# Optimization experiments

Measured on AMD Instinct MI355X. Metric: run time of the kernel, lower is better.

## Reference

```python
import jax, jax.numpy as jnp
import numpy as np

CONF_THRES = 0.5   # self.conf_thres
NMS_THRES = 0.5    # self.nms_thres
PRE_NMS = 2048     # candidates kept before pairwise IoU
MAX_DET = 300      # padded detections returned per image
MAX_WH = 4096.0    # class-offset trick so NMS is per-class
IMG_SIZE = 416.0   # self.img_size; boxes_scale (416,416)->(416,416) => scale 1


def xywh2xyxy(b):
    xy, wh = b[..., :2], b[..., 2:4]
    return jnp.concatenate([xy - wh * 0.5, xy + wh * 0.5], axis=-1)


def pairwise_iou(boxes):
    # boxes: [K,4] xyxy -> [K,K] IoU
    area = (boxes[:, 2] - boxes[:, 0]) * (boxes[:, 3] - boxes[:, 1])
    lt = jnp.maximum(boxes[:, None, :2], boxes[None, :, :2])
    rb = jnp.minimum(boxes[:, None, 2:], boxes[None, :, 2:])
    wh = jnp.clip(rb - lt, 0.0)
    inter = wh[..., 0] * wh[..., 1]
    return inter / (area[:, None] + area[None, :] - inter + 1e-16)


def nms_single(pred):
    # pred: [N,85] = xywh(4) + objectness(1) + class scores(80)
    boxes = xywh2xyxy(pred[:, :4])
    obj = pred[:, 4]
    cls_scores = pred[:, 5:] * obj[:, None]        # conf = obj * class prob
    conf = jnp.max(cls_scores, axis=-1)
    cls_id = jnp.argmax(cls_scores, axis=-1)
    valid = obj >= CONF_THRES                      # confidence threshold filter
    score = jnp.where(valid, conf, -1.0)

    order = jnp.argsort(-score)[:PRE_NMS]          # sort desc, keep top PRE_NMS
    boxes_s = boxes[order]
    score_s = score[order]
    cls_s = cls_id[order]
    valid_s = valid[order]

    # per-class NMS via coordinate offset by class id
    off = cls_s.astype(boxes_s.dtype) * MAX_WH
    iou = pairwise_iou(boxes_s + off[:, None])     # [PRE_NMS, PRE_NMS]

    def body(keep, i):
        suppressed = jnp.any(keep & (iou[:, i] > NMS_THRES))
        k = valid_s[i] & ~suppressed
        return keep.at[i].set(k), k

    keep, _ = jax.lax.scan(body, jnp.zeros(PRE_NMS, dtype=bool), jnp.arange(PRE_NMS))

    final_score = jnp.where(keep, score_s, -1.0)
    top = jnp.argsort(-final_score)[:MAX_DET]
    kb, ks, kc, km = boxes_s[top], score_s[top], cls_s[top], keep[top]

    scale = IMG_SIZE / 416.0                       # boxes_scale (identity here)
    det = jnp.concatenate(
        [kb * scale, ks[:, None], kc[:, None].astype(kb.dtype)], axis=-1)
    return jnp.where(km[:, None], det, 0.0)        # [MAX_DET, 6] padded


def setup_inputs() -> dict:
    key = jax.random.key(0)
    predictions = jax.random.uniform(key, (16, 10647, 85), dtype=jnp.float32)
    return {"predictions": predictions}


def reference(predictions):
    # detections per image: [x1,y1,x2,y2,score,class], zero-padded to MAX_DET
    return jax.vmap(nms_single)(predictions)  # [B, MAX_DET, 6]
```

## Files before the change

### kernel.cpp

```cpp
#include <hip/hip_runtime.h>
#include <hip/hip_bf16.h>
#include <stdint.h>

typedef unsigned long long u64;
typedef unsigned int u32;
typedef unsigned short u16;

#define NANCH 10647
#define NBATCH 16
#define NSORT 16384
#define NSEL 2048
#define NWORD 32
#define NCLS 80
#define CONF_T 0.5f
#define NMS_T 0.5f
#define MAXDET 300
#define MAXWH 4096.0f
#define CANDCAP 10688
#define PART 1344

__global__ __launch_bounds__(1024) void k_zero(u32* __restrict__ p, int nwords) {
    for (int i = threadIdx.x; i < nwords; i += 1024) p[i] = 0;
}

__global__ __launch_bounds__(256) void k_prep(const float* __restrict__ pred,
                                              u64* __restrict__ keys,
                                              float4* __restrict__ boxes,
                                              int* __restrict__ cls,
                                              float* __restrict__ score,
                                              u32* __restrict__ ghist) {
    __shared__ float sm[128 * 85];
    __shared__ u32 ph[256];
    int b = blockIdx.y;
    int a0 = blockIdx.x * 128;
    int na = NANCH - a0; if (na > 128) na = 128;
    const float* src = pred + ((size_t)b * NANCH + a0) * 85;
    int tot = na * 85;
    ph[threadIdx.x] = 0;
    {
        size_t srcaddr = (size_t)src;
        int shift = (int)((srcaddr & 15) >> 2);
        const float4* A = (const float4*)(srcaddr & ~(size_t)15);
        int nvec = (tot + shift + 3) >> 2;
        for (int j = threadIdx.x; j < nvec; j += 256) {
            float4 v = A[j];
            int base = 4 * j - shift;
            if (base >= 0 && base + 3 < tot) {
                sm[base] = v.x; sm[base + 1] = v.y;
                sm[base + 2] = v.z; sm[base + 3] = v.w;
            } else {
                if (base >= 0 && base < tot)     sm[base]     = v.x;
                if (base + 1 >= 0 && base + 1 < tot) sm[base + 1] = v.y;
                if (base + 2 >= 0 && base + 2 < tot) sm[base + 2] = v.z;
                if (base + 3 >= 0 && base + 3 < tot) sm[base + 3] = v.w;
            }
        }
    }
    __syncthreads();
    int t = threadIdx.x;
    u64 kk = 0;
    if (t < na) {
        const float* s = &sm[t * 85];
        float x = s[0], y = s[1], w = s[2], h = s[3], obj = s[4];
        float best = s[5] * obj; int arg = 0;
        #pragma unroll
        for (int c = 1; c < 80; ++c) {
            float v = s[5 + c] * obj;
            if (v > best) { best = v; arg = c; }
        }
        bool valid = obj >= CONF_T;
        float sc = valid ? best : -1.0f;
        int a = a0 + t;
        float4 bx;
        bx.x = x - w * 0.5f; bx.y = y - h * 0.5f;
        bx.z = x + w * 0.5f; bx.w = y + h * 0.5f;
        size_t o = (size_t)b * NANCH + a;
        boxes[o] = bx;
        cls[o] = arg;
        score[o] = sc;
        u32 u = __float_as_uint(sc);
        u32 v = (u & 0x80000000u) ? ~u : (u | 0x80000000u);
        u32 hi = ~v;
        kk = ((u64)hi << 32) | (u32)a;
        keys[(size_t)b * NSORT + a] = kk;
    }
    u32 bin = (t < na) ? (u32)(kk >> 56) : 0xFFFFFFFFu;
    int lane = t & 63;
    u64 rem = __ballot(t < na);
    while (rem) {
        int srcl = __ffsll((long long)rem) - 1;
        u32 lb = __shfl(bin, srcl);
        u64 same = __ballot(bin == lb) & rem;
        if (lane == srcl) atomicAdd(&ph[lb], (u32)__popcll(same));
        rem &= ~same;
    }
    __syncthreads();
    if (ph[threadIdx.x]) atomicAdd(&ghist[(size_t)b * 256 + threadIdx.x], ph[threadIdx.x]);
}

__global__ __launch_bounds__(1024) void k_scan(const u64* __restrict__ keys,
                                               const u32* __restrict__ ghist,
                                               u64* __restrict__ gsk,
                                               u64* __restrict__ gcand,
                                               u32* __restrict__ gcnt,
                                               u32* __restrict__ gcandcnt) {
    __shared__ u32 hist[256];
    __shared__ u32 hsc[256];
    __shared__ u32 s_D0;
    __shared__ u32 wcs[16], wcc[16];
    __shared__ u32 s_gbs, s_gbc;
    int b = blockIdx.y;
    int part = blockIdx.x;
    int tid = threadIdx.x;
    int lane = tid & 63, wv = tid >> 6;
    u64 below = (1ULL << lane) - 1ULL;
    const u64* KB = keys + (size_t)b * NSORT;

    if (tid < 256) hist[tid] = ghist[(size_t)b * 256 + tid];
    __syncthreads();
    if (tid < 64) {
        u32 h0 = hist[tid*4], h1 = hist[tid*4+1], h2 = hist[tid*4+2], h3 = hist[tid*4+3];
        u32 loc = h0 + h1 + h2 + h3;
        u32 p = loc;
        #pragma unroll
        for (int o = 1; o < 64; o <<= 1) { u32 t2 = __shfl_up(p, o); if (lane >= o) p += t2; }
        u32 base = p - loc;
        hsc[tid*4]   = base + h0;
        hsc[tid*4+1] = base + h0 + h1;
        hsc[tid*4+2] = base + h0 + h1 + h2;
        hsc[tid*4+3] = base + h0 + h1 + h2 + h3;
    }
    __syncthreads();
    if (tid < 256) {
        u32 inc = hsc[tid], cb = inc - hist[tid];
        if (cb < NSEL && NSEL <= inc) s_D0 = tid;
    }
    __syncthreads();
    u32 D0 = s_D0;

    u64 kk0 = 0, kk1 = 0;
    bool s0 = false, s1 = false, c0 = false, c1 = false;
    {
        int off = tid, i = part * PART + off;
        bool inb = (off < PART) && (i < NANCH);
        kk0 = inb ? KB[i] : 0ULL;
        u32 top = (u32)(kk0 >> 56);
        s0 = inb && (top < D0); c0 = inb && (top == D0);
    }
    {
        int off = 1024 + tid, i = part * PART + off;
        bool inb = (off < PART) && (i < NANCH);
        kk1 = inb ? KB[i] : 0ULL;
        u32 top = (u32)(kk1 >> 56);
        s1 = inb && (top < D0); c1 = inb && (top == D0);
    }
    u64 bs0 = __ballot(s0), bs1 = __ballot(s1);
    u64 bc0 = __ballot(c0), bc1 = __ballot(c1);
    if (lane == 0) {
        wcs[wv] = (u32)(__popcll(bs0) + __popcll(bs1));
        wcc[wv] = (u32)(__popcll(bc0) + __popcll(bc1));
    }
    __syncthreads();
    if (tid < 16) {
        u32 vs = wcs[tid], vc = wcc[tid];
        u32 ps = vs, pc = vc;
        #pragma unroll
        for (int o = 1; o < 16; o <<= 1) {
            u32 ts = __shfl_up(ps, o);
            u32 tc = __shfl_up(pc, o);
            if (tid >= o) { ps += ts; pc += tc; }
        }
        wcs[tid] = ps - vs;
        wcc[tid] = pc - vc;
        if (tid == 15) {
            s_gbs = ps ? atomicAdd(&gcnt[b], ps) : 0u;
            s_gbc = pc ? atomicAdd(&gcandcnt[b], pc) : 0u;
        }
    }
    __syncthreads();
    u64* SKB = gsk + (size_t)b * NSEL;
    u64* CDB = gcand + (size_t)b * CANDCAP;
    u32 base_s = s_gbs + wcs[wv];
    u32 base_c = s_gbc + wcc[wv];
    if (s0) SKB[base_s + __popcll(bs0 & below)] = kk0;
    if (s1) SKB[base_s + __popcll(bs0) + __popcll(bs1 & below)] = kk1;
    if (c0) CDB[base_c + __popcll(bc0 & below)] = kk0;
    if (c1) CDB[base_c + __popcll(bc0) + __popcll(bc1 & below)] = kk1;
}

__global__ __launch_bounds__(1024) void k_fin(const u64* __restrict__ gsk,
                                              const u64* __restrict__ gcand,
                                              const u32* __restrict__ gcnt,
                                              const u32* __restrict__ gcandcnt,
                                              u64* __restrict__ gskey) {
    __shared__ u64 sk[NSEL];
    __shared__ u64 cand[CANDCAP];
    __shared__ u32 hist[256];
    __shared__ u32 hsc[256];
    __shared__ u64 s_red[16];
    __shared__ u32 s_D, s_rank, s_cnt, s_cand;

    int b = blockIdx.x;
    int tid = threadIdx.x;
    int lane = tid & 63;
    u64 below = (1ULL << lane) - 1ULL;

    u32 skn = gcnt[b];
    u32 cn0 = gcandcnt[b];
    if (tid == 0) { s_cnt = skn; s_rank = NSEL - skn; s_cand = cn0; }
    for (int i = tid; i < NSEL; i += 1024)
        sk[i] = (i < (int)skn) ? gsk[(size_t)b * NSEL + i] : ~0ULL;
    for (u32 i = tid; i < cn0; i += 1024)
        cand[i] = gcand[(size_t)b * CANDCAP + i];
    __syncthreads();

    const int shifts2[5] = {48, 40, 32, 8, 0};
    for (int rr = 0; ; ++rr) {
        u32 cn = s_cand, r = s_rank;
        if (r == cn || rr == 5) {
            for (u32 i0 = 0; i0 < cn; i0 += 1024) {
                u32 i = i0 + tid;
                bool take = i < cn;
                u64 kk = take ? cand[i] : 0ULL;
                u64 bt = __ballot(take);
                u32 base = 0;
                if (lane == 0 && bt) base = atomicAdd(&s_cnt, (u32)__popcll(bt));
                base = __shfl(base, 0);
                if (take) sk[base + __popcll(bt & below)] = kk;
            }
            break;
        }
        if (r == 1) {
            u64 best = ~0ULL;
            for (u32 i = tid; i < cn; i += 1024) { u64 kk = cand[i]; if (kk < best) best = kk; }
            #pragma unroll
            for (int o = 32; o > 0; o >>= 1) {
                u64 other = __shfl_down(best, o);
                if (other < best) best = other;
            }
            if (lane == 0) s_red[tid >> 6] = best;
            __syncthreads();
            if (tid == 0) {
                u64 m = s_red[0];
                for (int w2 = 1; w2 < 16; ++w2) if (s_red[w2] < m) m = s_red[w2];
                sk[atomicAdd(&s_cnt, 1u)] = m;
            }
            break;
        }
        int shift = shifts2[rr];
        if (tid < 256) hist[tid] = 0;
        __syncthreads();
        for (u32 i = tid; i < cn; i += 1024)
            atomicAdd(&hist[(u32)(cand[i] >> shift) & 0xFFu], 1u);
        __syncthreads();
        if (tid < 64) {
            u32 h0 = hist[tid*4], h1 = hist[tid*4+1], h2 = hist[tid*4+2], h3 = hist[tid*4+3];
            u32 loc = h0 + h1 + h2 + h3;
            u32 p = loc;
            #pragma unroll
            for (int o = 1; o < 64; o <<= 1) { u32 t2 = __shfl_up(p, o); if (lane >= o) p += t2; }
            u32 base = p - loc;
            hsc[tid*4]   = base + h0;
            hsc[tid*4+1] = base + h0 + h1;
            hsc[tid*4+2] = base + h0 + h1 + h2;
            hsc[tid*4+3] = base + h0 + h1 + h2 + h3;
        }
        __syncthreads();
        if (tid < 256) {
            u32 inc = hsc[tid], cb = inc - hist[tid];
            if (cb < r && r <= inc) { s_D = tid; s_rank = r - cb; }
        }
        __syncthreads();
        u32 D = s_D;
        u64 vv[11]; bool vb[11];
        #pragma unroll
        for (int it = 0; it < 11; ++it) {
            u32 i = tid + it * 1024;
            vb[it] = (i < cn);
            vv[it] = vb[it] ? cand[i] : 0ULL;
        }
        __syncthreads();
        if (tid == 0) s_cand = 0;
        __syncthreads();
        #pragma unroll
        for (int it = 0; it < 11; ++it) {
            u32 dg = (u32)(vv[it] >> shift) & 0xFFu;
            bool tk = vb[it] && (dg < D);
            u64 bt = __ballot(tk);
            u32 base = 0;
            if (lane == 0 && bt) base = atomicAdd(&s_cnt, (u32)__popcll(bt));
            base = __shfl(base, 0);
            if (tk) sk[base + __popcll(bt & below)] = vv[it];
        }
        #pragma unroll
        for (int it = 0; it < 11; ++it) {
            u32 dg = (u32)(vv[it] >> shift) & 0xFFu;
            bool tk = vb[it] && (dg == D);
            u64 bt = __ballot(tk);
            u32 base = 0;
            if (lane == 0 && bt) base = atomicAdd(&s_cand, (u32)__popcll(bt));
            base = __shfl(base, 0);
            if (tk) cand[base + __popcll(bt & below)] = vv[it];
        }
        __syncthreads();
    }
    __syncthreads();

    {
        int w = tid >> 6, l = lane;
        int base = w * 128;
        u64 a = sk[base + l], c = sk[base + 64 + l];
        #pragma unroll
        for (int k = 2; k <= 128; k <<= 1) {
            for (int j = k >> 1; j > 0; j >>= 1) {
                if (j == 64) {
                    bool dir = (((base + l) & k) == 0);
                    u64 lo = a < c ? a : c;
                    u64 hi = a < c ? c : a;
                    a = dir ? lo : hi;
                    c = dir ? hi : lo;
                } else {
                    bool up_ = (l & j) != 0;
                    bool dira = (((base + l) & k) == 0);
                    bool dirc = (((base + 64 + l) & k) == 0);
                    u64 pa = __shfl_xor(a, j);
                    u64 pc = __shfl_xor(c, j);
                    a = (up_ == dira) ? (a > pa ? a : pa) : (a < pa ? a : pa);
                    c = (up_ == dirc) ? (c > pc ? c : pc) : (c < pc ? c : pc);
                }
            }
        }
        sk[base + l] = a; sk[base + 64 + l] = c;
        __syncthreads();
        for (int k = 256; k <= NSEL; k <<= 1) {
            for (int j = k >> 1; j >= 128; j >>= 1) {
                int n = tid;
                int i = ((n & ~(j - 1)) << 1) | (n & (j - 1));
                int l2 = i | j;
                u64 x = sk[i], y = sk[l2];
                bool up2 = ((i & k) == 0);
                if ((x > y) == up2) { sk[i] = y; sk[l2] = x; }
                __syncthreads();
            }
            a = sk[base + l]; c = sk[base + 64 + l];
            bool dirk = ((base & k) == 0);
            {
                u64 lo = a < c ? a : c;
                u64 hi = a < c ? c : a;
                a = dirk ? lo : hi;
                c = dirk ? hi : lo;
            }
            #pragma unroll
            for (int j = 32; j > 0; j >>= 1) {
                bool up_ = (l & j) != 0;
                u64 pa = __shfl_xor(a, j);
                u64 pc = __shfl_xor(c, j);
                a = (up_ == dirk) ? (a > pa ? a : pa) : (a < pa ? a : pa);
                c = (up_ == dirk) ? (c > pc ? c : pc) : (c < pc ? c : pc);
            }
            sk[base + l] = a; sk[base + 64 + l] = c;
            __syncthreads();
        }
    }

    for (int i = tid; i < NSEL; i += 1024) gskey[(size_t)b * NSEL + i] = sk[i];
}

__global__ __launch_bounds__(256) void k_gather(const u64* __restrict__ gskey,
                                                const float4* __restrict__ boxes,
                                                const int* __restrict__ cls,
                                                const float* __restrict__ score,
                                                float4* __restrict__ sel_box,
                                                float4* __restrict__ sel_sbox,
                                                float* __restrict__ sel_area,
                                                float* __restrict__ sel_score,
                                                int* __restrict__ sel_cls) {
    int b = blockIdx.y;
    int r = blockIdx.x * 256 + threadIdx.x;
    u64 key = gskey[(size_t)b * NSEL + r];
    int a = (int)(key & 0xFFFFFFFFu);
    if ((unsigned)a >= NANCH) a = 0;
    size_t src = (size_t)b * NANCH + a;
    float4 bx = boxes[src];
    int c = cls[src];
    float sc = score[src];
    float off = (float)c * MAXWH;
    float4 sb;
    sb.x = bx.x + off; sb.y = bx.y + off;
    sb.z = bx.z + off; sb.w = bx.w + off;
    float area = (sb.z - sb.x) * (sb.w - sb.y);
    size_t o = (size_t)b * NSEL + r;
    sel_box[o] = bx; sel_sbox[o] = sb; sel_area[o] = area;
    sel_score[o] = sc; sel_cls[o] = c;
}

__global__ __launch_bounds__(1024) void k_cnms(const float4* __restrict__ sel_sbox,
                                               const float* __restrict__ sel_area,
                                               const int* __restrict__ sel_cls,
                                               const float* __restrict__ sel_score,
                                               u64* __restrict__ gkeep) {
    __shared__ u16 wmem[16][NSEL];
    __shared__ u64 wkeep[16][NWORD];

    int b = blockIdx.y;
    int cg = blockIdx.x;
    int lane = threadIdx.x & 63, wv = threadIdx.x >> 6;
    int c = cg * 16 + wv;
    size_t bb = (size_t)b * NSEL;
    const int* CL = sel_cls + bb;
    const float* SC = sel_score + bb;
    u64 below = (1ULL << lane) - 1ULL;

    int n = 0;
    for (int ch = 0; ch < NWORD; ++ch) {
        int i = ch * 64 + lane;
        bool pred = (CL[i] == c) && (SC[i] >= 0.0f);
        u64 bal = __ballot(pred);
        if (pred) wmem[wv][n + __popcll(bal & below)] = (u16)i;
        n += __popcll(bal);
    }

    for (int c0 = 0; c0 < n; c0 += 64) {
        int chunkn = n - c0; if (chunkn > 64) chunkn = 64;
        bool mv = lane < chunkn;
        int q = mv ? (int)wmem[wv][c0 + lane] : 0;
        float4 bq = sel_sbox[bb + q];
        float aq = sel_area[bb + q];

        bool hit = false;
        for (int j = 0; j < c0; ++j) {
            if (!((wkeep[wv][j >> 6] >> (j & 63)) & 1ULL)) continue;
            int p = (int)wmem[wv][j];
            float4 bp = sel_sbox[bb + p];
            float ap = sel_area[bb + p];
            float ltx = fmaxf(bp.x, bq.x), lty = fmaxf(bp.y, bq.y);
            float rbx = fminf(bp.z, bq.z), rby = fminf(bp.w, bq.w);
            float ww = fmaxf(rbx - ltx, 0.0f), hh = fmaxf(rby - lty, 0.0f);
            float inter = ww * hh;
            hit = hit || (mv && (inter / (ap + aq - inter + 1e-16f) > NMS_T));
        }
        u64 avail = __ballot(mv && !hit);

        u64 Rt = 0;
        for (int t = 0; t < chunkn; ++t) {
            int p = (int)wmem[wv][c0 + t];
            float4 bp = sel_sbox[bb + p];
            float ap = sel_area[bb + p];
            float ltx = fmaxf(bp.x, bq.x), lty = fmaxf(bp.y, bq.y);
            float rbx = fminf(bp.z, bq.z), rby = fminf(bp.w, bq.w);
            float ww = fmaxf(rbx - ltx, 0.0f), hh = fmaxf(rby - lty, 0.0f);
            float inter = ww * hh;
            u64 row = __ballot(mv && (inter / (ap + aq - inter + 1e-16f) > NMS_T));
            if (lane == t) Rt = row;
        }

        u64 U = avail, kept = 0;
        while (U) {
            bool inU = ((U >> lane) & 1ULL) != 0ULL;
            u64 newk = __ballot(inU && ((Rt & U & below) == 0ULL));
            u64 killed = __ballot((Rt & newk) != 0ULL);
            kept |= newk;
            U &= ~(newk | killed);
        }
        if (lane == 0) wkeep[wv][c0 >> 6] = kept;
        if ((kept >> lane) & 1ULL)
            atomicOr(&gkeep[(size_t)b * NWORD + (q >> 6)], 1ULL << (q & 63));
    }
}

__global__ __launch_bounds__(64) void k_out(const u64* __restrict__ gkeep,
                                            const float4* __restrict__ sel_box,
                                            const float* __restrict__ sel_score,
                                            const int* __restrict__ sel_cls,
                                            float* __restrict__ out) {
    int b = blockIdx.x;
    int lane = threadIdx.x;
    const float* SC = sel_score + (size_t)b * NSEL;
    u64 kreg = (lane < NWORD) ? gkeep[(size_t)b * NWORD + lane] : 0ULL;

    int cnt = (lane < NWORD) ? __popcll(kreg) : 0;
    int pre = cnt;
    #pragma unroll
    for (int dd = 1; dd < 64; dd <<= 1) {
        int o = __shfl_up(pre, dd);
        if (lane >= dd) pre += o;
    }
    int total = __shfl(pre, 63);
    int base = pre - cnt;
    float* OUT = out + (size_t)b * MAXDET * 6;
    if (lane < NWORD) {
        u64 m = kreg;
        int rr = 0;
        while (m) {
            int t = __ffsll((long long)m) - 1;
            m &= m - 1;
            int slot = base + rr; ++rr;
            if (slot < MAXDET) {
                int i = lane * 64 + t;
                size_t src = (size_t)b * NSEL + i;
                float4 bx = sel_box[src];
                float sc = SC[i];
                int c = sel_cls[src];
                float* o6 = OUT + slot * 6;
                o6[0] = bx.x; o6[1] = bx.y; o6[2] = bx.z; o6[3] = bx.w;
                o6[4] = sc; o6[5] = (float)c;
            }
        }
    }
    int start = total > MAXDET ? MAXDET : total;
    for (int s = start + lane; s < MAXDET; s += 64) {
        float* o6 = OUT + s * 6;
        o6[0] = 0.0f; o6[1] = 0.0f; o6[2] = 0.0f;
        o6[3] = 0.0f; o6[4] = 0.0f; o6[5] = 0.0f;
    }
}

extern "C" void kernel_launch(void* const* d_in, const int* in_sizes, int n_in,
                              void* d_out, int out_size, void* d_ws, size_t ws_size,
                              hipStream_t stream) {
    const float* pred = (const float*)d_in[0];
    float* out = (float*)d_out;

    char* ws = (char*)d_ws;
    size_t off = 0;
    auto alloc = [&](size_t bytes) -> void* {
        void* p = ws + off;
        off += (bytes + 255) & ~(size_t)255;
        return p;
    };

    u64*    keys      = (u64*)   alloc((size_t)NBATCH * NSORT * 8);
    float4* boxes     = (float4*)alloc((size_t)NBATCH * NANCH * 16);
    int*    cls       = (int*)   alloc((size_t)NBATCH * NANCH * 4);
    float*  score     = (float*) alloc((size_t)NBATCH * NANCH * 4);
    float4* sel_box   = (float4*)alloc((size_t)NBATCH * NSEL * 16);
    float4* sel_sbox  = (float4*)alloc((size_t)NBATCH * NSEL * 16);
    float*  sel_area  = (float*) alloc((size_t)NBATCH * NSEL * 4);
    float*  sel_score = (float*) alloc((size_t)NBATCH * NSEL * 4);
    int*    sel_cls   = (int*)   alloc((size_t)NBATCH * NSEL * 4);
    u64*    gsk       = (u64*)   alloc((size_t)NBATCH * NSEL * 8);
    u64*    gcand     = (u64*)   alloc((size_t)NBATCH * CANDCAP * 8);
    u64*    gskey     = (u64*)   alloc((size_t)NBATCH * NSEL * 8);
    u64*    gkeep     = (u64*)   alloc((size_t)NBATCH * NWORD * 8);
    u32*    ghist     = (u32*)   alloc((size_t)NBATCH * 256 * 4);
    u32*    gcnt      = (u32*)   alloc((size_t)NBATCH * 4);
    u32*    gcandcnt  = (u32*)   alloc((size_t)NBATCH * 4);

    size_t zbytes = (char*)(gcandcnt + NBATCH) - (char*)gkeep;
    k_zero<<<1, 1024, 0, stream>>>((u32*)gkeep, (int)(zbytes / 4));

    dim3 g1((NANCH + 127) / 128, NBATCH);
    k_prep<<<g1, 256, 0, stream>>>(pred, keys, boxes, cls, score, ghist);

    dim3 g2(8, NBATCH);
    k_scan<<<g2, 1024, 0, stream>>>(keys, ghist, gsk, gcand, gcnt, gcandcnt);

    k_fin<<<NBATCH, 1024, 0, stream>>>(gsk, gcand, gcnt, gcandcnt, gskey);

    dim3 g4(8, NBATCH);
    k_gather<<<g4, 256, 0, stream>>>(gskey, boxes, cls, score,
                                     sel_box, sel_sbox, sel_area,
                                     sel_score, sel_cls);

    dim3 g5(5, NBATCH);
    k_cnms<<<g5, 1024, 0, stream>>>(sel_sbox, sel_area, sel_cls, sel_score, gkeep);

    k_out<<<NBATCH, 64, 0, stream>>>(gkeep, sel_box, sel_score, sel_cls, out);
}
```

Before: 105.7 us.

## Drop zero and gather kernels; use per-block histograms and per-part slices

Removes the k_zero and k_gather launches. Histograms are now written per block and summed in k_scan, which replaces global atomics. Each scan part writes into its own fixed slice, so no atomic counters are needed. k_fin zeroes the keep mask and compacts the slices, and k_cnms/k_out read boxes and classes indirectly through the sorted keys, with the score decoded from the key. This cuts launch count and global traffic, in exchange for indirect gathers inside the NMS inner loops and a serial 84-way histogram sum per bin.

After: 122.0 us. 1.15x slower.

```diff
diff --git a/kernel.cpp b/kernel.cpp
--- a/kernel.cpp
+++ b/kernel.cpp
@@ -18,17 +18,19 @@
 #define MAXWH 4096.0f
 #define CANDCAP 10688
 #define PART 1344
-
-__global__ __launch_bounds__(1024) void k_zero(u32* __restrict__ p, int nwords) {
-    for (int i = threadIdx.x; i < nwords; i += 1024) p[i] = 0;
+#define NBLK1 84
+
+__device__ __forceinline__ float dec_score(u64 key) {
+    u32 v = ~(u32)(key >> 32);
+    u32 u = (v & 0x80000000u) ? (v & 0x7FFFFFFFu) : ~v;
+    return __uint_as_float(u);
 }
 
 __global__ __launch_bounds__(256) void k_prep(const float* __restrict__ pred,
                                               u64* __restrict__ keys,
                                               float4* __restrict__ boxes,
                                               int* __restrict__ cls,
-                                              float* __restrict__ score,
-                                              u32* __restrict__ ghist) {
+                                              u32* __restrict__ bhist) {
     __shared__ float sm[128 * 85];
     __shared__ u32 ph[256];
     int b = blockIdx.y;
@@ -49,7 +51,7 @@
                 sm[base] = v.x; sm[base + 1] = v.y;
                 sm[base + 2] = v.z; sm[base + 3] = v.w;
             } else {
-                if (base >= 0 && base < tot)     sm[base]     = v.x;
+                if (base >= 0 && base < tot)         sm[base]     = v.x;
                 if (base + 1 >= 0 && base + 1 < tot) sm[base + 1] = v.y;
                 if (base + 2 >= 0 && base + 2 < tot) sm[base + 2] = v.z;
                 if (base + 3 >= 0 && base + 3 < tot) sm[base + 3] = v.w;
@@ -77,7 +79,6 @@
         size_t o = (size_t)b * NANCH + a;
         boxes[o] = bx;
         cls[o] = arg;
-        score[o] = sc;
         u32 u = __float_as_uint(sc);
         u32 v = (u & 0x80000000u) ? ~u : (u | 0x80000000u);
         u32 hi = ~v;
@@ -95,20 +96,18 @@
         rem &= ~same;
     }
     __syncthreads();
-    if (ph[threadIdx.x]) atomicAdd(&ghist[(size_t)b * 256 + threadIdx.x], ph[threadIdx.x]);
+    bhist[(((size_t)b * NBLK1) + blockIdx.x) * 256 + threadIdx.x] = ph[threadIdx.x];
 }
 
 __global__ __launch_bounds__(1024) void k_scan(const u64* __restrict__ keys,
-                                               const u32* __restrict__ ghist,
-                                               u64* __restrict__ gsk,
-                                               u64* __restrict__ gcand,
-                                               u32* __restrict__ gcnt,
-                                               u32* __restrict__ gcandcnt) {
+                                               const u32* __restrict__ bhist,
+                                               u64* __restrict__ gslice,
+                                               uint2* __restrict__ gpart) {
     __shared__ u32 hist[256];
     __shared__ u32 hsc[256];
     __shared__ u32 s_D0;
     __shared__ u32 wcs[16], wcc[16];
-    __shared__ u32 s_gbs, s_gbc;
+    __shared__ u32 s_tc;
     int b = blockIdx.y;
     int part = blockIdx.x;
     int tid = threadIdx.x;
@@ -116,7 +115,12 @@
     u64 below = (1ULL << lane) - 1ULL;
     const u64* KB = keys + (size_t)b * NSORT;
 
-    if (tid < 256) hist[tid] = ghist[(size_t)b * 256 + tid];
+    if (tid < 256) {
+        u32 h = 0;
+        const u32* BH = bhist + (size_t)b * NBLK1 * 256 + tid;
+        for (int j = 0; j < NBLK1; ++j) h += BH[(size_t)j * 256];
+        hist[tid] = h;
+    }
     __syncthreads();
     if (tid < 64) {
         u32 h0 = hist[tid*4], h1 = hist[tid*4+1], h2 = hist[tid*4+2], h3 = hist[tid*4+3];
@@ -173,31 +177,30 @@
         wcs[tid] = ps - vs;
         wcc[tid] = pc - vc;
         if (tid == 15) {
-            s_gbs = ps ? atomicAdd(&gcnt[b], ps) : 0u;
-            s_gbc = pc ? atomicAdd(&gcandcnt[b], pc) : 0u;
-        }
-    }
-    __syncthreads();
-    u64* SKB = gsk + (size_t)b * NSEL;
-    u64* CDB = gcand + (size_t)b * CANDCAP;
-    u32 base_s = s_gbs + wcs[wv];
-    u32 base_c = s_gbc + wcc[wv];
-    if (s0) SKB[base_s + __popcll(bs0 & below)] = kk0;
-    if (s1) SKB[base_s + __popcll(bs0) + __popcll(bs1 & below)] = kk1;
-    if (c0) CDB[base_c + __popcll(bc0 & below)] = kk0;
-    if (c1) CDB[base_c + __popcll(bc0) + __popcll(bc1 & below)] = kk1;
-}
-
-__global__ __launch_bounds__(1024) void k_fin(const u64* __restrict__ gsk,
-                                              const u64* __restrict__ gcand,
-                                              const u32* __restrict__ gcnt,
-                                              const u32* __restrict__ gcandcnt,
-                                              u64* __restrict__ gskey) {
+            s_tc = pc;
+            gpart[(size_t)b * 8 + part] = make_uint2(ps, pc);
+        }
+    }
+    __syncthreads();
+    u64* SL = gslice + ((size_t)b * 8 + part) * (size_t)PART;
+    u32 base_s = wcs[wv];
+    u32 base_c = (u32)PART - s_tc + wcc[wv];
+    if (s0) SL[base_s + __popcll(bs0 & below)] = kk0;
+    if (s1) SL[base_s + __popcll(bs0) + __popcll(bs1 & below)] = kk1;
+    if (c0) SL[base_c + __popcll(bc0 & below)] = kk0;
+    if (c1) SL[base_c + __popcll(bc0) + __popcll(bc1 & below)] = kk1;
+}
+
+__global__ __launch_bounds__(1024) void k_fin(const u64* __restrict__ gslice,
+                                              const uint2* __restrict__ gpart,
+                                              u64* __restrict__ gskey,
+                                              u64* __restrict__ gkeep) {
     __shared__ u64 sk[NSEL];
     __shared__ u64 cand[CANDCAP];
     __shared__ u32 hist[256];
     __shared__ u32 hsc[256];
     __shared__ u64 s_red[16];
+    __shared__ u32 ssA[8], ccA[8], soff[9], coff[9];
     __shared__ u32 s_D, s_rank, s_cnt, s_cand;
 
     int b = blockIdx.x;
@@ -205,13 +208,23 @@
     int lane = tid & 63;
     u64 below = (1ULL << lane) - 1ULL;
 
-    u32 skn = gcnt[b];
-    u32 cn0 = gcandcnt[b];
-    if (tid == 0) { s_cnt = skn; s_rank = NSEL - skn; s_cand = cn0; }
-    for (int i = tid; i < NSEL; i += 1024)
-        sk[i] = (i < (int)skn) ? gsk[(size_t)b * NSEL + i] : ~0ULL;
-    for (u32 i = tid; i < cn0; i += 1024)
-        cand[i] = gcand[(size_t)b * CANDCAP + i];
+    if (tid < 8) { uint2 v = gpart[(size_t)b * 8 + tid]; ssA[tid] = v.x; ccA[tid] = v.y; }
+    for (int i = tid; i < NSEL; i += 1024) sk[i] = ~0ULL;
+    __syncthreads();
+    if (tid == 0) {
+        u32 a = 0, c2 = 0;
+        for (int j = 0; j < 8; ++j) { soff[j] = a; a += ssA[j]; coff[j] = c2; c2 += ccA[j]; }
+        soff[8] = a; coff[8] = c2;
+        s_cnt = a; s_rank = NSEL - a; s_cand = c2;
+    }
+    __syncthreads();
+    for (int j = 0; j < 8; ++j) {
+        const u64* SL = gslice + ((size_t)b * 8 + j) * (size_t)PART;
+        u32 ns = ssA[j], nc = ccA[j];
+        u32 so = soff[j], co = coff[j];
+        for (u32 i = tid; i < ns; i += 1024) sk[so + i] = SL[i];
+        for (u32 i = tid; i < nc; i += 1024) cand[co + i] = SL[PART - nc + i];
+    }
     __syncthreads();
 
     const int shifts2[5] = {48, 40, 32, 8, 0};
@@ -364,40 +377,12 @@
     }
 
     for (int i = tid; i < NSEL; i += 1024) gskey[(size_t)b * NSEL + i] = sk[i];
-}
-
-__global__ __launch_bounds__(256) void k_gather(const u64* __restrict__ gskey,
-                                                const float4* __restrict__ boxes,
-                                                const int* __restrict__ cls,
-                                                const float* __restrict__ score,
-                                                float4* __restrict__ sel_box,
-                                                float4* __restrict__ sel_sbox,
-                                                float* __restrict__ sel_area,
-                                                float* __restrict__ sel_score,
-                                                int* __restrict__ sel_cls) {
-    int b = blockIdx.y;
-    int r = blockIdx.x * 256 + threadIdx.x;
-    u64 key = gskey[(size_t)b * NSEL + r];
-    int a = (int)(key & 0xFFFFFFFFu);
-    if ((unsigned)a >= NANCH) a = 0;
-    size_t src = (size_t)b * NANCH + a;
-    float4 bx = boxes[src];
-    int c = cls[src];
-    float sc = score[src];
-    float off = (float)c * MAXWH;
-    float4 sb;
-    sb.x = bx.x + off; sb.y = bx.y + off;
-    sb.z = bx.z + off; sb.w = bx.w + off;
-    float area = (sb.z - sb.x) * (sb.w - sb.y);
-    size_t o = (size_t)b * NSEL + r;
-    sel_box[o] = bx; sel_sbox[o] = sb; sel_area[o] = area;
-    sel_score[o] = sc; sel_cls[o] = c;
-}
-
-__global__ __launch_bounds__(1024) void k_cnms(const float4* __restrict__ sel_sbox,
-                                               const float* __restrict__ sel_area,
-                                               const int* __restrict__ sel_cls,
-                                               const float* __restrict__ sel_score,
+    if (tid < NWORD) gkeep[(size_t)b * NWORD + tid] = 0ULL;
+}
+
+__global__ __launch_bounds__(1024) void k_cnms(const u64* __restrict__ gskey,
+                                               const float4* __restrict__ boxes,
+                                               const int* __restrict__ cls,
                                                u64* __restrict__ gkeep) {
     __shared__ u16 wmem[16][NSEL];
     __shared__ u64 wkeep[16][NWORD];
@@ -406,15 +391,20 @@
     int cg = blockIdx.x;
     int lane = threadIdx.x & 63, wv = threadIdx.x >> 6;
     int c = cg * 16 + wv;
-    size_t bb = (size_t)b * NSEL;
-    const int* CL = sel_cls + bb;
-    const float* SC = sel_score + bb;
+    const u64* KY = gskey + (size_t)b * NSEL;
+    const float4* BX = boxes + (size_t)b * NANCH;
+    const int* CL = cls + (size_t)b * NANCH;
     u64 below = (1ULL << lane) - 1ULL;
+    float off = (float)c * MAXWH;
 
     int n = 0;
     for (int ch = 0; ch < NWORD; ++ch) {
         int i = ch * 64 + lane;
-        bool pred = (CL[i] == c) && (SC[i] >= 0.0f);
+        u64 key = KY[i];
+        bool valid = (key >> 63) == 0ULL;
+        int a = (int)(key & 0xFFFFFFFFu);
+        int ci = valid ? CL[a] : -1;
+        bool pred = (ci == c);
         u64 bal = __ballot(pred);
         if (pred) wmem[wv][n + __popcll(bal & below)] = (u16)i;
         n += __popcll(bal);
@@ -424,33 +414,45 @@
         int chunkn = n - c0; if (chunkn > 64) chunkn = 64;
         bool mv = lane < chunkn;
         int q = mv ? (int)wmem[wv][c0 + lane] : 0;
-        float4 bq = sel_sbox[bb + q];
-        float aq = sel_area[bb + q];
+        int aq = (int)(KY[q] & 0xFFFFFFFFu);
+        float4 b4 = BX[aq];
+        float4 bq;
+        bq.x = b4.x + off; bq.y = b4.y + off;
+        bq.z = b4.z + off; bq.w = b4.w + off;
+        float aqr = (bq.z - bq.x) * (bq.w - bq.y);
 
         bool hit = false;
         for (int j = 0; j < c0; ++j) {
             if (!((wkeep[wv][j >> 6] >> (j & 63)) & 1ULL)) continue;
             int p = (int)wmem[wv][j];
-            float4 bp = sel_sbox[bb + p];
-            float ap = sel_area[bb + p];
+            int ap = (int)(KY[p] & 0xFFFFFFFFu);
+            float4 p4 = BX[ap];
+            float4 bp;
+            bp.x = p4.x + off; bp.y = p4.y + off;
+            bp.z = p4.z + off; bp.w = p4.w + off;
+            float apr = (bp.z - bp.x) * (bp.w - bp.y);
             float ltx = fmaxf(bp.x, bq.x), lty = fmaxf(bp.y, bq.y);
             float rbx = fminf(bp.z, bq.z), rby = fminf(bp.w, bq.w);
             float ww = fmaxf(rbx - ltx, 0.0f), hh = fmaxf(rby - lty, 0.0f);
             float inter = ww * hh;
-            hit = hit || (mv && (inter / (ap + aq - inter + 1e-16f) > NMS_T));
+            hit = hit || (mv && (inter / (apr + aqr - inter + 1e-16f) > NMS_T));
         }
         u64 avail = __ballot(mv && !hit);
 
         u64 Rt = 0;
         for (int t = 0; t < chunkn; ++t) {
             int p = (int)wmem[wv][c0 + t];
-            float4 bp = sel_sbox[bb + p];
-            float ap = sel_area[bb + p];
+            int ap = (int)(KY[p] & 0xFFFFFFFFu);
+            float4 p4 = BX[ap];
+            float4 bp;
+            bp.x = p4.x + off; bp.y = p4.y + off;
+            bp.z = p4.z + off; bp.w = p4.w + off;
+            float apr = (bp.z - bp.x) * (bp.w - bp.y);
             float ltx = fmaxf(bp.x, bq.x), lty = fmaxf(bp.y, bq.y);
             float rbx = fminf(bp.z, bq.z), rby = fminf(bp.w, bq.w);
             float ww = fmaxf(rbx - ltx, 0.0f), hh = fmaxf(rby - lty, 0.0f);
             float inter = ww * hh;
-            u64 row = __ballot(mv && (inter / (ap + aq - inter + 1e-16f) > NMS_T));
+            u64 row = __ballot(mv && (inter / (apr + aqr - inter + 1e-16f) > NMS_T));
             if (lane == t) Rt = row;
         }
 
@@ -469,13 +471,13 @@
 }
 
 __global__ __launch_bounds__(64) void k_out(const u64* __restrict__ gkeep,
-                                            const float4* __restrict__ sel_box,
-                                            const float* __restrict__ sel_score,
-                                            const int* __restrict__ sel_cls,
+                                            const u64* __restrict__ gskey,
+                                            const float4* __restrict__ boxes,
+                                            const int* __restrict__ cls,
                                             float* __restrict__ out) {
     int b = blockIdx.x;
     int lane = threadIdx.x;
-    const float* SC = sel_score + (size_t)b * NSEL;
+    const u64* KY = gskey + (size_t)b * NSEL;
     u64 kreg = (lane < NWORD) ? gkeep[(size_t)b * NWORD + lane] : 0ULL;
 
     int cnt = (lane < NWORD) ? __popcll(kreg) : 0;
@@ -497,10 +499,12 @@
             int slot = base + rr; ++rr;
             if (slot < MAXDET) {
                 int i = lane * 64 + t;
-                size_t src = (size_t)b * NSEL + i;
-                float4 bx = sel_box[src];
-                float sc = SC[i];
-                int c = sel_cls[src];
+                u64 key = KY[i];
+                int a = (int)(key & 0xFFFFFFFFu);
+                if ((unsigned)a >= NANCH) a = 0;
+                float4 bx = boxes[(size_t)b * NANCH + a];
+                int c = cls[(size_t)b * NANCH + a];
+                float sc = dec_score(key);
                 float* o6 = OUT + slot * 6;
                 o6[0] = bx.x; o6[1] = bx.y; o6[2] = bx.z; o6[3] = bx.w;
                 o6[4] = sc; o6[5] = (float)c;
@@ -529,41 +533,25 @@
         return p;
     };
 
-    u64*    keys      = (u64*)   alloc((size_t)NBATCH * NSORT * 8);
-    float4* boxes     = (float4*)alloc((size_t)NBATCH * NANCH * 16);
-    int*    cls       = (int*)   alloc((size_t)NBATCH * NANCH * 4);
-    float*  score     = (float*) alloc((size_t)NBATCH * NANCH * 4);
-    float4* sel_box   = (float4*)alloc((size_t)NBATCH * NSEL * 16);
-    float4* sel_sbox  = (float4*)alloc((size_t)NBATCH * NSEL * 16);
-    float*  sel_area  = (float*) alloc((size_t)NBATCH * NSEL * 4);
-    float*  sel_score = (float*) alloc((size_t)NBATCH * NSEL * 4);
-    int*    sel_cls   = (int*)   alloc((size_t)NBATCH * NSEL * 4);
-    u64*    gsk       = (u64*)   alloc((size_t)NBATCH * NSEL * 8);
-    u64*    gcand     = (u64*)   alloc((size_t)NBATCH * CANDCAP * 8);
-    u64*    gskey     = (u64*)   alloc((size_t)NBATCH * NSEL * 8);
-    u64*    gkeep     = (u64*)   alloc((size_t)NBATCH * NWORD * 8);
-    u32*    ghist     = (u32*)   alloc((size_t)NBATCH * 256 * 4);
-    u32*    gcnt      = (u32*)   alloc((size_t)NBATCH * 4);
-    u32*    gcandcnt  = (u32*)   alloc((size_t)NBATCH * 4);
-
-    size_t zbytes = (char*)(gcandcnt + NBATCH) - (char*)gkeep;
-    k_zero<<<1, 1024, 0, stream>>>((u32*)gkeep, (int)(zbytes / 4));
-
-    dim3 g1((NANCH + 127) / 128, NBATCH);
-    k_prep<<<g1, 256, 0, stream>>>(pred, keys, boxes, cls, score, ghist);
+    u64*    keys   = (u64*)   alloc((size_t)NBATCH * NSORT * 8);
+    float4* boxes  = (float4*)alloc((size_t)NBATCH * NANCH * 16);
+    int*    cls    = (int*)   alloc((size_t)NBATCH * NANCH * 4);
+    u32*    bhist  = (u32*)   alloc((size_t)NBATCH * NBLK1 * 256 * 4);
+    u64*    gslice = (u64*)   alloc((size_t)NBATCH * 8 * PART * 8);
+    uint2*  gpart  = (uint2*) alloc((size_t)NBATCH * 8 * 8);
+    u64*    gskey  = (u64*)   alloc((size_t)NBATCH * NSEL * 8);
+    u64*    gkeep  = (u64*)   alloc((size_t)NBATCH * NWORD * 8);
+
+    dim3 g1(NBLK1, NBATCH);
+    k_prep<<<g1, 256, 0, stream>>>(pred, keys, boxes, cls, bhist);
 
     dim3 g2(8, NBATCH);
-    k_scan<<<g2, 1024, 0, stream>>>(keys, ghist, gsk, gcand, gcnt, gcandcnt);
-
-    k_fin<<<NBATCH, 1024, 0, stream>>>(gsk, gcand, gcnt, gcandcnt, gskey);
-
-    dim3 g4(8, NBATCH);
-    k_gather<<<g4, 256, 0, stream>>>(gskey, boxes, cls, score,
-                                     sel_box, sel_sbox, sel_area,
-                                     sel_score, sel_cls);
-
-    dim3 g5(5, NBATCH);
-    k_cnms<<<g5, 1024, 0, stream>>>(sel_sbox, sel_area, sel_cls, sel_score, gkeep);
-
-    k_out<<<NBATCH, 64, 0, stream>>>(gkeep, sel_box, sel_score, sel_cls, out);
-}
+    k_scan<<<g2, 1024, 0, stream>>>(keys, bhist, gslice, gpart);
+
+    k_fin<<<NBATCH, 1024, 0, stream>>>(gslice, gpart, gskey, gkeep);
+
+    dim3 g4(5, NBATCH);
+    k_cnms<<<g4, 1024, 0, stream>>>(gskey, boxes, cls, gkeep);
+
+    k_out<<<NBATCH, 64, 0, stream>>>(gkeep, gskey, boxes, cls, out);
+}
```

## Replace global atomics with per-block histograms and slices, drop zero kernel

Applied to the files above, without the earlier changes.

Per-block radix histograms are written to a scratch array and summed in k_scan, and each scan partition writes its selected and candidate keys into a private slice with a per-partition count, in place of atomic counters. k_fin compacts the slices using prefix sums of those counts and zeroes the keep mask itself, so the separate k_zero launch is removed. The score array is dropped and scores are decoded from the sort key. This removes one launch, the global atomics and the zeroing dependency, in exchange for extra histogram reads (84 per bin) and a serial offset loop in k_fin.

Result: faster. 103.0 us (-2.5%).

```diff
diff --git a/kernel.cpp b/kernel.cpp
--- a/kernel.cpp
+++ b/kernel.cpp
@@ -18,17 +18,19 @@
 #define MAXWH 4096.0f
 #define CANDCAP 10688
 #define PART 1344
-
-__global__ __launch_bounds__(1024) void k_zero(u32* __restrict__ p, int nwords) {
-    for (int i = threadIdx.x; i < nwords; i += 1024) p[i] = 0;
+#define NBLK1 84
+
+__device__ __forceinline__ float dec_score(u64 key) {
+    u32 v = ~(u32)(key >> 32);
+    u32 u = (v & 0x80000000u) ? (v & 0x7FFFFFFFu) : ~v;
+    return __uint_as_float(u);
 }
 
 __global__ __launch_bounds__(256) void k_prep(const float* __restrict__ pred,
                                               u64* __restrict__ keys,
                                               float4* __restrict__ boxes,
                                               int* __restrict__ cls,
-                                              float* __restrict__ score,
-                                              u32* __restrict__ ghist) {
+                                              u32* __restrict__ bhist) {
     __shared__ float sm[128 * 85];
     __shared__ u32 ph[256];
     int b = blockIdx.y;
@@ -49,7 +51,7 @@
                 sm[base] = v.x; sm[base + 1] = v.y;
                 sm[base + 2] = v.z; sm[base + 3] = v.w;
             } else {
-                if (base >= 0 && base < tot)     sm[base]     = v.x;
+                if (base >= 0 && base < tot)         sm[base]     = v.x;
                 if (base + 1 >= 0 && base + 1 < tot) sm[base + 1] = v.y;
                 if (base + 2 >= 0 && base + 2 < tot) sm[base + 2] = v.z;
                 if (base + 3 >= 0 && base + 3 < tot) sm[base + 3] = v.w;
@@ -77,7 +79,6 @@
         size_t o = (size_t)b * NANCH + a;
         boxes[o] = bx;
         cls[o] = arg;
-        score[o] = sc;
         u32 u = __float_as_uint(sc);
         u32 v = (u & 0x80000000u) ? ~u : (u | 0x80000000u);
         u32 hi = ~v;
@@ -95,20 +96,18 @@
         rem &= ~same;
     }
     __syncthreads();
-    if (ph[threadIdx.x]) atomicAdd(&ghist[(size_t)b * 256 + threadIdx.x], ph[threadIdx.x]);
+    bhist[(((size_t)b * NBLK1) + blockIdx.x) * 256 + threadIdx.x] = ph[threadIdx.x];
 }
 
 __global__ __launch_bounds__(1024) void k_scan(const u64* __restrict__ keys,
-                                               const u32* __restrict__ ghist,
-                                               u64* __restrict__ gsk,
-                                               u64* __restrict__ gcand,
-                                               u32* __restrict__ gcnt,
-                                               u32* __restrict__ gcandcnt) {
+                                               const u32* __restrict__ bhist,
+                                               u64* __restrict__ gslice,
+                                               uint2* __restrict__ gpart) {
     __shared__ u32 hist[256];
     __shared__ u32 hsc[256];
     __shared__ u32 s_D0;
     __shared__ u32 wcs[16], wcc[16];
-    __shared__ u32 s_gbs, s_gbc;
+    __shared__ u32 s_tc;
     int b = blockIdx.y;
     int part = blockIdx.x;
     int tid = threadIdx.x;
@@ -116,7 +115,12 @@
     u64 below = (1ULL << lane) - 1ULL;
     const u64* KB = keys + (size_t)b * NSORT;
 
-    if (tid < 256) hist[tid] = ghist[(size_t)b * 256 + tid];
+    if (tid < 256) {
+        u32 h = 0;
+        const u32* BH = bhist + (size_t)b * NBLK1 * 256 + tid;
+        for (int j = 0; j < NBLK1; ++j) h += BH[(size_t)j * 256];
+        hist[tid] = h;
+    }
     __syncthreads();
     if (tid < 64) {
         u32 h0 = hist[tid*4], h1 = hist[tid*4+1], h2 = hist[tid*4+2], h3 = hist[tid*4+3];
@@ -173,31 +177,30 @@
         wcs[tid] = ps - vs;
         wcc[tid] = pc - vc;
         if (tid == 15) {
-            s_gbs = ps ? atomicAdd(&gcnt[b], ps) : 0u;
-            s_gbc = pc ? atomicAdd(&gcandcnt[b], pc) : 0u;
-        }
-    }
-    __syncthreads();
-    u64* SKB = gsk + (size_t)b * NSEL;
-    u64* CDB = gcand + (size_t)b * CANDCAP;
-    u32 base_s = s_gbs + wcs[wv];
-    u32 base_c = s_gbc + wcc[wv];
-    if (s0) SKB[base_s + __popcll(bs0 & below)] = kk0;
-    if (s1) SKB[base_s + __popcll(bs0) + __popcll(bs1 & below)] = kk1;
-    if (c0) CDB[base_c + __popcll(bc0 & below)] = kk0;
-    if (c1) CDB[base_c + __popcll(bc0) + __popcll(bc1 & below)] = kk1;
-}
-
-__global__ __launch_bounds__(1024) void k_fin(const u64* __restrict__ gsk,
-                                              const u64* __restrict__ gcand,
-                                              const u32* __restrict__ gcnt,
-                                              const u32* __restrict__ gcandcnt,
-                                              u64* __restrict__ gskey) {
+            s_tc = pc;
+            gpart[(size_t)b * 8 + part] = make_uint2(ps, pc);
+        }
+    }
+    __syncthreads();
+    u64* SL = gslice + ((size_t)b * 8 + part) * (size_t)PART;
+    u32 base_s = wcs[wv];
+    u32 base_c = (u32)PART - s_tc + wcc[wv];
+    if (s0) SL[base_s + __popcll(bs0 & below)] = kk0;
+    if (s1) SL[base_s + __popcll(bs0) + __popcll(bs1 & below)] = kk1;
+    if (c0) SL[base_c + __popcll(bc0 & below)] = kk0;
+    if (c1) SL[base_c + __popcll(bc0) + __popcll(bc1 & below)] = kk1;
+}
+
+__global__ __launch_bounds__(1024) void k_fin(const u64* __restrict__ gslice,
+                                              const uint2* __restrict__ gpart,
+                                              u64* __restrict__ gskey,
+                                              u64* __restrict__ gkeep) {
     __shared__ u64 sk[NSEL];
     __shared__ u64 cand[CANDCAP];
     __shared__ u32 hist[256];
     __shared__ u32 hsc[256];
     __shared__ u64 s_red[16];
+    __shared__ u32 ssA[8], ccA[8], soff[9], coff[9];
     __shared__ u32 s_D, s_rank, s_cnt, s_cand;
 
     int b = blockIdx.x;
@@ -205,13 +208,23 @@
     int lane = tid & 63;
     u64 below = (1ULL << lane) - 1ULL;
 
-    u32 skn = gcnt[b];
-    u32 cn0 = gcandcnt[b];
-    if (tid == 0) { s_cnt = skn; s_rank = NSEL - skn; s_cand = cn0; }
-    for (int i = tid; i < NSEL; i += 1024)
-        sk[i] = (i < (int)skn) ? gsk[(size_t)b * NSEL + i] : ~0ULL;
-    for (u32 i = tid; i < cn0; i += 1024)
-        cand[i] = gcand[(size_t)b * CANDCAP + i];
+    if (tid < 8) { uint2 v = gpart[(size_t)b * 8 + tid]; ssA[tid] = v.x; ccA[tid] = v.y; }
+    for (int i = tid; i < NSEL; i += 1024) sk[i] = ~0ULL;
+    __syncthreads();
+    if (tid == 0) {
+        u32 a = 0, c2 = 0;
+        for (int j = 0; j < 8; ++j) { soff[j] = a; a += ssA[j]; coff[j] = c2; c2 += ccA[j]; }
+        soff[8] = a; coff[8] = c2;
+        s_cnt = a; s_rank = NSEL - a; s_cand = c2;
+    }
+    __syncthreads();
+    for (int j = 0; j < 8; ++j) {
+        const u64* SL = gslice + ((size_t)b * 8 + j) * (size_t)PART;
+        u32 ns = ssA[j], nc = ccA[j];
+        u32 so = soff[j], co = coff[j];
+        for (u32 i = tid; i < ns; i += 1024) sk[so + i] = SL[i];
+        for (u32 i = tid; i < nc; i += 1024) cand[co + i] = SL[PART - nc + i];
+    }
     __syncthreads();
 
     const int shifts2[5] = {48, 40, 32, 8, 0};
@@ -364,12 +377,12 @@
     }
 
     for (int i = tid; i < NSEL; i += 1024) gskey[(size_t)b * NSEL + i] = sk[i];
+    if (tid < NWORD) gkeep[(size_t)b * NWORD + tid] = 0ULL;
 }
 
 __global__ __launch_bounds__(256) void k_gather(const u64* __restrict__ gskey,
                                                 const float4* __restrict__ boxes,
                                                 const int* __restrict__ cls,
-                                                const float* __restrict__ score,
                                                 float4* __restrict__ sel_box,
                                                 float4* __restrict__ sel_sbox,
                                                 float* __restrict__ sel_area,
@@ -383,7 +396,7 @@
     size_t src = (size_t)b * NANCH + a;
     float4 bx = boxes[src];
     int c = cls[src];
-    float sc = score[src];
+    float sc = dec_score(key);
     float off = (float)c * MAXWH;
     float4 sb;
     sb.x = bx.x + off; sb.y = bx.y + off;
@@ -532,33 +545,27 @@
     u64*    keys      = (u64*)   alloc((size_t)NBATCH * NSORT * 8);
     float4* boxes     = (float4*)alloc((size_t)NBATCH * NANCH * 16);
     int*    cls       = (int*)   alloc((size_t)NBATCH * NANCH * 4);
-    float*  score     = (float*) alloc((size_t)NBATCH * NANCH * 4);
+    u32*    bhist     = (u32*)   alloc((size_t)NBATCH * NBLK1 * 256 * 4);
+    u64*    gslice    = (u64*)   alloc((size_t)NBATCH * 8 * PART * 8);
+    uint2*  gpart     = (uint2*) alloc((size_t)NBATCH * 8 * 8);
+    u64*    gskey     = (u64*)   alloc((size_t)NBATCH * NSEL * 8);
+    u64*    gkeep     = (u64*)   alloc((size_t)NBATCH * NWORD * 8);
     float4* sel_box   = (float4*)alloc((size_t)NBATCH * NSEL * 16);
     float4* sel_sbox  = (float4*)alloc((size_t)NBATCH * NSEL * 16);
     float*  sel_area  = (float*) alloc((size_t)NBATCH * NSEL * 4);
     float*  sel_score = (float*) alloc((size_t)NBATCH * NSEL * 4);
     int*    sel_cls   = (int*)   alloc((size_t)NBATCH * NSEL * 4);
-    u64*    gsk       = (u64*)   alloc((size_t)NBATCH * NSEL * 8);
-    u64*    gcand     = (u64*)   alloc((size_t)NBATCH * CANDCAP * 8);
-    u64*    gskey     = (u64*)   alloc((size_t)NBATCH * NSEL * 8);
-    u64*    gkeep     = (u64*)   alloc((size_t)NBATCH * NWORD * 8);
-    u32*    ghist     = (u32*)   alloc((size_t)NBATCH * 256 * 4);
-    u32*    gcnt      = (u32*)   alloc((size_t)NBATCH * 4);
-    u32*    gcandcnt  = (u32*)   alloc((size_t)NBATCH * 4);
-
-    size_t zbytes = (char*)(gcandcnt + NBATCH) - (char*)gkeep;
-    k_zero<<<1, 1024, 0, stream>>>((u32*)gkeep, (int)(zbytes / 4));
-
-    dim3 g1((NANCH + 127) / 128, NBATCH);
-    k_prep<<<g1, 256, 0, stream>>>(pred, keys, boxes, cls, score, ghist);
+
+    dim3 g1(NBLK1, NBATCH);
+    k_prep<<<g1, 256, 0, stream>>>(pred, keys, boxes, cls, bhist);
 
     dim3 g2(8, NBATCH);
-    k_scan<<<g2, 1024, 0, stream>>>(keys, ghist, gsk, gcand, gcnt, gcandcnt);
-
-    k_fin<<<NBATCH, 1024, 0, stream>>>(gsk, gcand, gcnt, gcandcnt, gskey);
+    k_scan<<<g2, 1024, 0, stream>>>(keys, bhist, gslice, gpart);
+
+    k_fin<<<NBATCH, 1024, 0, stream>>>(gslice, gpart, gskey, gkeep);
 
     dim3 g4(8, NBATCH);
-    k_gather<<<g4, 256, 0, stream>>>(gskey, boxes, cls, score,
+    k_gather<<<g4, 256, 0, stream>>>(gskey, boxes, cls,
                                      sel_box, sel_sbox, sel_area,
                                      sel_score, sel_cls);
 
```
